# Performance work log

Measured on AMD Instinct MI355X. Metric: run time of the kernel, lower is better.

Reference implementation:

```python
import jax, jax.numpy as jnp
import numpy as np

B, T, E, H, VF, C = 4, 8192, 512, 8, 2, 256
KD = E // H          # key dim per head = 64
HD = E * VF // H     # value head dim = 128


def _rel_pos():
    decay = np.log(1.0 - 2.0 ** (-5.0 - np.arange(H, dtype=np.float64)))  # [H]
    ang = 1.0 / (10000 ** np.linspace(0, 1, KD // 2))
    ang = np.repeat(ang, 2)                                  # [KD]
    idx = np.arange(T)
    sin = np.sin(idx[:, None] * ang[None, :]).astype(np.float32)
    cos = np.cos(idx[:, None] * ang[None, :]).astype(np.float32)
    bi = np.arange(C)
    diff = bi[:, None] - bi[None, :]
    m = np.where(diff >= 0, np.exp(decay[:, None, None] * diff), 0.0)  # [H,C,C]
    last = m[:, -1]                                          # [H,C]
    vid = (last / last.sum(-1, keepdims=True))[:, :, None]   # [H,C,1]
    scale = np.sqrt(m.sum(-1, keepdims=True))                # [H,C,1]
    mask = (m / scale).astype(np.float32)
    cross_decay = np.exp(decay * C)[:, None, None].astype(np.float32)  # [H,1,1]
    qid = np.exp(decay[:, None] * (bi + 1))[:, :, None]      # [H,C,1]
    qid = (qid / (scale / last.sum(-1)[:, None, None])).astype(np.float32)
    return sin, cos, mask, cross_decay, qid, vid.astype(np.float32)


def setup_inputs() -> dict:
    key = jax.random.key(0)
    ks = jax.random.split(key, 6)
    sin, cos, mask, cross_decay, qid, vid = _rel_pos()
    s = 0.02
    return {
        'x': jax.random.normal(ks[0], (B, T, E), jnp.float32),
        'sin': jnp.asarray(sin), 'cos': jnp.asarray(cos),
        'mask': jnp.asarray(mask), 'cross_decay': jnp.asarray(cross_decay),
        'query_inner_decay': jnp.asarray(qid), 'value_inner_decay': jnp.asarray(vid),
        'Wq': jax.random.normal(ks[1], (E, E), jnp.float32) * s,
        'Wk': jax.random.normal(ks[2], (E, E), jnp.float32) * s,
        'Wv': jax.random.normal(ks[3], (E, E * VF), jnp.float32) * s,
        'Wg': jax.random.normal(ks[4], (E, E * VF), jnp.float32) * s,
        'Wo': jax.random.normal(ks[5], (E * VF, E), jnp.float32) * s,
    }


def _rotate_every_two(x):
    x1, x2 = x[..., ::2], x[..., 1::2]
    return jnp.stack((-x2, x1), axis=-1).reshape(x.shape)


def _theta_shift(x, sin, cos):
    return x * cos + _rotate_every_two(x) * sin


def reference(x, sin, cos, mask, cross_decay, query_inner_decay, value_inner_decay, Wq, Wk, Wv, Wg, Wo):
    Bz, Tl, _ = x.shape
    q = (x @ Wq).reshape(Bz, Tl, H, KD).transpose(0, 2, 1, 3)               # [B,H,T,KD]
    k = ((x @ Wk) * (KD ** -0.5)).reshape(Bz, Tl, H, KD).transpose(0, 2, 1, 3)
    v = x @ Wv                                                              # [B,T,E*VF]
    g = x @ Wg
    qr = _theta_shift(q, sin, cos)
    kr = _theta_shift(k, sin, cos)

    NC = Tl // C
    qr = qr.reshape(Bz, H, NC, C, KD).transpose(0, 2, 1, 3, 4)              # [B,NC,H,C,KD]
    kr = kr.reshape(Bz, H, NC, C, KD).transpose(0, 2, 1, 3, 4)
    vc = v.reshape(Bz, NC, C, H, HD).transpose(0, 1, 3, 2, 4)               # [B,NC,H,C,HD]

    qk = jnp.einsum('bnhck,bnhdk->bnhcd', qr, kr) * mask                    # decay-masked intra-chunk
    inner_scale = jnp.clip(jax.lax.stop_gradient(jnp.abs(qk)).sum(-1, keepdims=True), 1.0, None)
    qk = qk / inner_scale
    inner_output = jnp.einsum('bnhcd,bnhde->bnhce', qk, vc)                 # [B,NC,H,C,HD]

    kv = jnp.einsum('bnhck,bnhcd->bnhkd', kr, vc * value_inner_decay)       # [B,NC,H,KD,HD]

    def step(carry, kv_i):
        kv_state, kv_scale = carry
        out = (kv_state / kv_scale, kv_scale)
        kv_state = kv_state * cross_decay + kv_i
        kv_scale = jnp.clip(
            jax.lax.stop_gradient(jnp.abs(kv_state)).sum(-2, keepdims=True).max(-1, keepdims=True),
            1.0, None)
        return (kv_state, kv_scale), out

    kv_state0 = jnp.zeros((Bz, H, KD, HD), x.dtype)
    kv_scale0 = jnp.ones((Bz, H, 1, 1), x.dtype)
    _, (kv_recurrent, cross_scale) = jax.lax.scan(step, (kv_state0, kv_scale0), jnp.swapaxes(kv, 0, 1))
    kv_recurrent = jnp.swapaxes(kv_recurrent, 0, 1)                         # [B,NC,H,KD,HD]
    cross_scale = jnp.swapaxes(cross_scale, 0, 1)                           # [B,NC,H,1,1]

    all_scale = jnp.maximum(inner_scale, cross_scale)
    cross_output = jnp.einsum('bnhck,bnhkd->bnhcd', qr * query_inner_decay, kv_recurrent)
    output = inner_output / (all_scale / inner_scale) + cross_output / (all_scale / cross_scale)
    output = output.transpose(0, 1, 3, 2, 4)                                # [B,NC,C,H,HD]
    # group_norm: RMSNorm over head_dim, no affine
    output = output * jax.lax.rsqrt(jnp.mean(output ** 2, -1, keepdims=True) + 1e-6)
    output = output.reshape(Bz, Tl, H * HD)
    output = jax.nn.silu(g) * output
    return output @ Wo
```

## Files before the change

### kernel.cpp

```cpp
#include <hip/hip_runtime.h>
#include <hip/hip_bf16.h>
#include <cmath>

#define Bz 4
#define Tt 8192
#define Ee 512
#define Hh 8
#define Cc 256
#define KD 64
#define HD 128
#define NC 32
#define EV 1024
#define Mrows (Bz*Tt)

typedef unsigned short u16;
typedef __attribute__((ext_vector_type(4))) float f32x4;
typedef __attribute__((ext_vector_type(8))) short s16x8;

__device__ __forceinline__ u16 f2b(float f) {
    __hip_bfloat16 h = __float2bfloat16(f);
    return *reinterpret_cast<u16*>(&h);
}
__device__ __forceinline__ float b2f(u16 u) {
    union { unsigned u; float f; } v; v.u = ((unsigned)u) << 16;
    return v.f;
}
#define MFMA16(a, b, c) __builtin_amdgcn_mfma_f32_16x16x32_bf16((a), (b), (c), 0, 0, 0)

__device__ __forceinline__ void glds16(const u16* g, u16* l) {
    __builtin_amdgcn_global_load_lds(
        (const __attribute__((address_space(1))) unsigned int*)g,
        (__attribute__((address_space(3))) unsigned int*)l,
        16, 0, 0);
}

__device__ __forceinline__ size_t fpk(int row, int k, int K) {
    return (size_t)(row >> 4) * (K * 16) + (k >> 5) * 512 + ((k >> 3) & 3) * 128 +
           (row & 15) * 8 + (k & 7);
}

__global__ __launch_bounds__(256) void cast_x_k(const float* __restrict__ x,
                                                u16* __restrict__ xb) {
    size_t i = ((size_t)blockIdx.x * 256 + threadIdx.x) * 4;
    float4 v = *(const float4*)(x + i);
    int m = (int)(i >> 9), e = (int)(i & 511);
    ushort4 o;
    o.x = f2b(v.x); o.y = f2b(v.y); o.z = f2b(v.z); o.w = f2b(v.w);
    *(ushort4*)(xb + fpk(m, e, 512)) = o;
}

__global__ __launch_bounds__(256) void cast_mask_k(const float* __restrict__ m,
                                                   u16* __restrict__ mb) {
    size_t i = ((size_t)blockIdx.x * 256 + threadIdx.x) * 4;
    float4 v = *(const float4*)(m + i);
    ushort4 o;
    o.x = f2b(v.x); o.y = f2b(v.y); o.z = f2b(v.z); o.w = f2b(v.w);
    *(ushort4*)(mb + i) = o;
}

__global__ __launch_bounds__(256) void castT_k(const float* __restrict__ W,
                                               u16* __restrict__ Wt,
                                               int K, int N, float scale) {
    __shared__ float tile[32][33];
    int k0 = blockIdx.y * 32, n0 = blockIdx.x * 32;
    int r = threadIdx.x >> 3, c4 = (threadIdx.x & 7) * 4;
    float4 v = *(const float4*)(W + (size_t)(k0 + r) * N + n0 + c4);
    tile[r][c4] = v.x; tile[r][c4 + 1] = v.y; tile[r][c4 + 2] = v.z; tile[r][c4 + 3] = v.w;
    __syncthreads();
    ushort4 o;
    o.x = f2b(tile[c4 + 0][r] * scale);
    o.y = f2b(tile[c4 + 1][r] * scale);
    o.z = f2b(tile[c4 + 2][r] * scale);
    o.w = f2b(tile[c4 + 3][r] * scale);
    *(ushort4*)(Wt + fpk(n0 + r, k0 + c4, K)) = o;
}

template <int EPI>
__global__ __launch_bounds__(256) void gemm_mfma(const u16* __restrict__ A,
                                                 const u16* __restrict__ Bt,
                                                 void* __restrict__ Cout,
                                                 int K, int N,
                                                 const float* __restrict__ sn,
                                                 const float* __restrict__ cs) {
    __shared__ __align__(16) u16 pool[20480];
    u16 (*lds)[8192] = (u16(*)[8192])pool;
    int tid = threadIdx.x;
    int lane = tid & 63, wid = tid >> 6;
    int cL = lane & 15, quad = lane >> 4;
    int M0 = blockIdx.y * 8, N0 = blockIdx.x * 8;
    int m0 = blockIdx.y * 128 + (wid & 1) * 64;
    int n0 = blockIdx.x * 128 + (wid >> 1) * 64;
    const int KT = K * 16;
    const int NK = K >> 5;

#define STAGE(buf, kc) do {                                                        \
        size_t kofs = (size_t)(kc) * 512 + lane * 8;                               \
        glds16(A  + (size_t)(M0 + wid * 2    ) * KT + kofs,                        \
               &lds[buf][(wid * 2    ) * 512]);                                    \
        glds16(A  + (size_t)(M0 + wid * 2 + 1) * KT + kofs,                        \
               &lds[buf][(wid * 2 + 1) * 512]);                                    \
        glds16(Bt + (size_t)(N0 + wid * 2    ) * KT + kofs,                        \
               &lds[buf][4096 + (wid * 2    ) * 512]);                             \
        glds16(Bt + (size_t)(N0 + wid * 2 + 1) * KT + kofs,                        \
               &lds[buf][4096 + (wid * 2 + 1) * 512]);                             \
    } while (0)

    STAGE(0, 0);
    __syncthreads();

    f32x4 acc[4][4] = {};
    int mh = (wid & 1) * 4, nh = (wid >> 1) * 4;
    for (int kc = 0; kc < NK; ++kc) {
        int cur = kc & 1;
        if (kc + 1 < NK) STAGE(cur ^ 1, kc + 1);
        s16x8 af[4], bfr[4];
        int fo = quad * 128 + cL * 8;
        #pragma unroll
        for (int mt = 0; mt < 4; ++mt)
            af[mt] = *(const s16x8*)(&lds[cur][(mh + mt) * 512 + fo]);
        #pragma unroll
        for (int nt = 0; nt < 4; ++nt)
            bfr[nt] = *(const s16x8*)(&lds[cur][4096 + (nh + nt) * 512 + fo]);
        #pragma unroll
        for (int mt = 0; mt < 4; ++mt)
            #pragma unroll
            for (int nt = 0; nt < 4; ++nt)
                acc[mt][nt] = MFMA16(af[mt], bfr[nt], acc[mt][nt]);
        __syncthreads();
    }
#undef STAGE
    u16* ep = pool + wid * 5120;

    if (EPI == 0) {
        u16* dst = (u16*)Cout;
        int b = m0 >> 13, h = n0 >> 6, tb = m0 & 8191;
        #pragma unroll
        for (int mt = 0; mt < 4; ++mt)
            #pragma unroll
            for (int nt = 0; nt < 4; ++nt)
                #pragma unroll
                for (int i = 0; i < 4; ++i) {
                    int mrow = mt * 16 + quad * 4 + i;
                    int n = n0 + nt * 16 + cL;
                    float v = acc[mt][nt][i];
                    float p = __shfl_xor(v, 1, 64);
                    int t = tb + mrow, kd = n & 63;
                    float c1 = cs[t * 64 + kd], s1 = sn[t * 64 + kd];
                    float o = (n & 1) ? (v * c1 + p * s1) : (v * c1 - p * s1);
                    ep[mrow * 80 + nt * 16 + cL] = f2b(o);
                }
        u16* dstbh = dst + (size_t)(b * 8 + h) * 524288;
        #pragma unroll
        for (int g2 = 0; g2 < 4; ++g2)
            #pragma unroll
            for (int pass = 0; pass < 2; ++pass) {
                int kcol = pass * 32 + quad * 8;
                s16x8 vv = *(const s16x8*)(ep + (g2 * 16 + cL) * 80 + kcol);
                *(s16x8*)(dstbh + fpk(tb + g2 * 16 + cL, kcol, 64)) = vv;
            }
    } else if (EPI == 1) {
        u16* vt = (u16*)Cout;
        #pragma unroll
        for (int mt = 0; mt < 4; ++mt)
            #pragma unroll
            for (int nt = 0; nt < 4; ++nt) {
                int m = m0 + mt * 16 + quad * 4;
                int n = n0 + nt * 16 + cL;
                int b = m >> 13, t = m & 8191;
                int nn = t >> 8, ccc = t & 255;
                int h = n >> 7, e = n & 127;
                ushort4 pk;
                pk.x = f2b(acc[mt][nt][0]);
                pk.y = f2b(acc[mt][nt][1]);
                pk.z = f2b(acc[mt][nt][2]);
                pk.w = f2b(acc[mt][nt][3]);
                *(ushort4*)(vt + (((size_t)((b * 8 + h) * 32 + nn)) << 15) +
                            fpk(e, ccc, 256)) = pk;
            }
    } else if (EPI == 2) {
        u16* dst = (u16*)Cout;
        #pragma unroll
        for (int mt = 0; mt < 4; ++mt)
            #pragma unroll
            for (int nt = 0; nt < 4; ++nt)
                #pragma unroll
                for (int i = 0; i < 4; ++i)
                    ep[(mt * 16 + quad * 4 + i) * 80 + nt * 16 + cL] =
                        f2b(acc[mt][nt][i]);
        #pragma unroll
        for (int g2 = 0; g2 < 4; ++g2)
            #pragma unroll
            for (int pass = 0; pass < 2; ++pass) {
                int ncol = pass * 32 + quad * 8;
                s16x8 vv = *(const s16x8*)(ep + (g2 * 16 + cL) * 80 + ncol);
                *(s16x8*)(dst + fpk(m0 + g2 * 16 + cL, n0 + ncol, N)) = vv;
            }
    } else {
        float* dst = (float*)Cout;
        #pragma unroll
        for (int mt = 0; mt < 4; ++mt)
            #pragma unroll
            for (int nt = 0; nt < 4; ++nt)
                #pragma unroll
                for (int i = 0; i < 4; ++i)
                    dst[(size_t)(m0 + mt * 16 + quad * 4 + i) * N + n0 + nt * 16 + cL] =
                        acc[mt][nt][i];
    }
}

__global__ __launch_bounds__(256) void attn_mfma(const u16* __restrict__ qr,
                                                 const u16* __restrict__ kr,
                                                 const u16* __restrict__ vt,
                                                 const u16* __restrict__ maskb,
                                                 u16* __restrict__ ATT,
                                                 float* __restrict__ iscale_g) {
    __shared__ __align__(16) u16 Ss[64][264];
    __shared__ float partial[4][64];
    __shared__ float sInvL[64];
    int p = blockIdx.x;
    int g = (p & 7) | ((p >> 5) << 3);
    int rtile = (p >> 3) & 3;
    int h = g & 7; int n = (g >> 3) & 31; int b = g >> 8;
    int tid = threadIdx.x, lane = tid & 63, w = tid >> 6;
    int cL = lane & 15, quad = lane >> 4;

    size_t qf_bh = (size_t)(b * 8 + h) * 524288;
    f32x4 acc[4][4] = {};
    if (w <= rtile) {
        const u16* Qb = qr + qf_bh + (size_t)(n * 16 + rtile * 4) * 1024;
        const u16* Kb = kr + qf_bh + (size_t)(n * 16 + w * 4) * 1024;
        #pragma unroll
        for (int kt = 0; kt < 2; ++kt) {
            s16x8 af[4], bfr[4];
            size_t ko = (size_t)kt * 512 + quad * 128 + cL * 8;
            #pragma unroll
            for (int mt = 0; mt < 4; ++mt)
                af[mt] = *(const s16x8*)(Qb + (size_t)mt * 1024 + ko);
            #pragma unroll
            for (int nt = 0; nt < 4; ++nt)
                bfr[nt] = *(const s16x8*)(Kb + (size_t)nt * 1024 + ko);
            #pragma unroll
            for (int mt = 0; mt < 4; ++mt)
                #pragma unroll
                for (int nt = 0; nt < 4; ++nt)
                    acc[mt][nt] = MFMA16(af[mt], bfr[nt], acc[mt][nt]);
        }
    }
    float rs[4][4] = {};
    if (w <= rtile) {
        const u16* mb = maskb + ((size_t)h << 16);
        #pragma unroll
        for (int mt = 0; mt < 4; ++mt)
            #pragma unroll
            for (int nt = 0; nt < 4; ++nt)
                #pragma unroll
                for (int i = 0; i < 4; ++i) {
                    int r = rtile * 64 + mt * 16 + quad * 4 + i;
                    int d = w * 64 + nt * 16 + cL;
                    float s = acc[mt][nt][i] * b2f(mb[r * 256 + d]);
                    Ss[mt * 16 + quad * 4 + i][w * 64 + nt * 16 + cL] = f2b(s);
                    rs[mt][i] += fabsf(s);
                }
    }
    #pragma unroll
    for (int mt = 0; mt < 4; ++mt)
        #pragma unroll
        for (int i = 0; i < 4; ++i) {
            float v = rs[mt][i];
            v += __shfl_xor(v, 1, 16);
            v += __shfl_xor(v, 2, 16);
            v += __shfl_xor(v, 4, 16);
            v += __shfl_xor(v, 8, 16);
            if (cL == 0) partial[w][mt * 16 + quad * 4 + i] = v;
        }
    __syncthreads();
    if (tid < 64) {
        float tot = partial[0][tid] + partial[1][tid] + partial[2][tid] + partial[3][tid];
        tot = fmaxf(tot, 1.f);
        iscale_g[((size_t)((b * 32 + n) * 8 + h)) * 256 + rtile * 64 + tid] = tot;
        sInvL[tid] = 1.f / tot;
    }
    __syncthreads();

    f32x4 o[8] = {};
    const u16* Vb = vt + (((size_t)((b * 8 + h) * 32 + n)) << 15);
    int kmax = 2 * (rtile + 1);
    for (int kt = 0; kt < kmax; ++kt) {
        s16x8 a = *(const s16x8*)(&Ss[w * 16 + cL][kt * 32 + quad * 8]);
        #pragma unroll
        for (int nt = 0; nt < 8; ++nt) {
            s16x8 bv = *(const s16x8*)(Vb + (size_t)nt * 4096 + kt * 512 +
                                       quad * 128 + cL * 8);
            o[nt] = MFMA16(a, bv, o[nt]);
        }
    }
    #pragma unroll
    for (int nt = 0; nt < 8; ++nt)
        #pragma unroll
        for (int i = 0; i < 4; ++i) {
            int r = quad * 4 + i;
            Ss[w * 16 + r][nt * 16 + cL] = f2b(o[nt][i] * sInvL[w * 16 + r]);
        }
    size_t obase = ((size_t)b * 8192 + n * 256 + rtile * 64) * 1024 + h * 128;
    #pragma unroll
    for (int pass = 0; pass < 4; ++pass) {
        int e = pass * 32 + quad * 8;
        s16x8 vv = *(const s16x8*)(&Ss[w * 16 + cL][e]);
        *(s16x8*)(ATT + obase + (size_t)(w * 16 + cL) * 1024 + e) = vv;
    }
}

__global__ __launch_bounds__(256) void chunkkv_mfma(const u16* __restrict__ kr,
                                                    const u16* __restrict__ vt,
                                                    const float* __restrict__ vid,
                                                    float* __restrict__ kvT) {
    __shared__ u16 KtL[64][264];
    int bid = blockIdx.x;
    int h = bid & 7; bid >>= 3;
    int n = bid & 31; int b = bid >> 5;
    int tid = threadIdx.x, lane = tid & 63, w = tid >> 6;
    int cL = lane & 15, quad = lane >> 4;
    size_t qf_bh = (size_t)(b * 8 + h) * 524288;
    {
        int c = tid;
        const u16* rp = kr + qf_bh + (size_t)(n * 16 + (c >> 4)) * 1024 + (c & 15) * 8;
        #pragma unroll
        for (int u = 0; u < 8; ++u) {
            s16x8 vv = *(const s16x8*)(rp + (u >> 2) * 512 + (u & 3) * 128);
            #pragma unroll
            for (int j = 0; j < 8; ++j) KtL[u * 8 + j][c] = (u16)vv[j];
        }
    }
    __syncthreads();
    const u16* Vb = vt + (((size_t)((b * 8 + h) * 32 + n)) << 15);
    f32x4 acc[2][4] = {};
    for (int kt = 0; kt < 8; ++kt) {
        float vidv[8];
        #pragma unroll
        for (int j = 0; j < 8; ++j) vidv[j] = vid[h * 256 + kt * 32 + quad * 8 + j];
        s16x8 af[2];
        #pragma unroll
        for (int mt = 0; mt < 2; ++mt) {
            s16x8 raw = *(const s16x8*)(Vb + (size_t)(w * 2 + mt) * 4096 +
                                        kt * 512 + quad * 128 + cL * 8);
            #pragma unroll
            for (int j = 0; j < 8; ++j)
                af[mt][j] = (short)f2b(b2f((u16)raw[j]) * vidv[j]);
        }
        #pragma unroll
        for (int nt = 0; nt < 4; ++nt) {
            s16x8 bv = *(const s16x8*)(&KtL[nt * 16 + cL][kt * 32 + quad * 8]);
            #pragma unroll
            for (int mt = 0; mt < 2; ++mt) acc[mt][nt] = MFMA16(af[mt], bv, acc[mt][nt]);
        }
    }
    float* out = kvT + ((size_t)((b * 32 + n) * 8 + h)) * 8192;
    #pragma unroll
    for (int mt = 0; mt < 2; ++mt)
        #pragma unroll
        for (int nt = 0; nt < 4; ++nt)
            #pragma unroll
            for (int i = 0; i < 4; ++i)
                out[(w * 32 + mt * 16 + quad * 4 + i) * 64 + nt * 16 + cL] = acc[mt][nt][i];
}

__global__ __launch_bounds__(256) void scan_par(const float* __restrict__ kvT,
                                                u16* __restrict__ kvrecb,
                                                const float* __restrict__ cdv,
                                                float* __restrict__ cscale) {
    int bid = blockIdx.x;
    int n = bid & 31; bid >>= 5;
    int h = bid & 7; int b = bid >> 3;
    int tid = threadIdx.x, lane = tid & 63, g = tid >> 6;
    float cd = cdv[h];
    float st[32], cur[32], nxt[32];
    #pragma unroll
    for (int i = 0; i < 32; ++i) { st[i] = 0.f; nxt[i] = 0.f; }
    if (n > 0) {
        size_t base0 = ((size_t)((b * 32) * 8 + h)) * 8192;
        #pragma unroll
        for (int i = 0; i < 32; ++i) cur[i] = kvT[base0 + (g + 4 * i) * 64 + lane];
    }
    for (int j = 0; j < n; ++j) {
        if (j + 1 < n) {
            size_t basen = ((size_t)((b * 32 + j + 1) * 8 + h)) * 8192;
            #pragma unroll
            for (int i = 0; i < 32; ++i) nxt[i] = kvT[basen + (g + 4 * i) * 64 + lane];
        }
        #pragma unroll
        for (int i = 0; i < 32; ++i) st[i] = st[i] * cd + cur[i];
        #pragma unroll
        for (int i = 0; i < 32; ++i) cur[i] = nxt[i];
    }
    __shared__ float esum[128];
    __shared__ float sSc;
    #pragma unroll
    for (int i = 0; i < 32; ++i) {
        float s = fabsf(st[i]);
        s += __shfl_xor(s, 1, 64);
        s += __shfl_xor(s, 2, 64);
        s += __shfl_xor(s, 4, 64);
        s += __shfl_xor(s, 8, 64);
        s += __shfl_xor(s, 16, 64);
        s += __shfl_xor(s, 32, 64);
        if (lane == 0) esum[g + 4 * i] = s;
    }
    __syncthreads();
    if (tid < 64) {
        float m1 = fmaxf(esum[tid], esum[tid + 64]);
        m1 = fmaxf(m1, __shfl_xor(m1, 1, 64));
        m1 = fmaxf(m1, __shfl_xor(m1, 2, 64));
        m1 = fmaxf(m1, __shfl_xor(m1, 4, 64));
        m1 = fmaxf(m1, __shfl_xor(m1, 8, 64));
        m1 = fmaxf(m1, __shfl_xor(m1, 16, 64));
        m1 = fmaxf(m1, __shfl_xor(m1, 32, 64));
        if (tid == 0) sSc = fmaxf(m1, 1.f);
    }
    __syncthreads();
    float scale = sSc;
    float inv = 1.f / scale;
    size_t baseN = ((size_t)((b * 32 + n) * 8 + h)) * 8192;
    #pragma unroll
    for (int i = 0; i < 32; ++i) {
        int e = g + 4 * i;
        kvrecb[baseN + ((size_t)(lane >> 3) * 128 + e) * 8 + (lane & 7)] = f2b(st[i] * inv);
    }
    if (tid == 0) cscale[(b * 32 + n) * 8 + h] = scale;
}

__global__ __launch_bounds__(256) void cross_mfma(const u16* __restrict__ qr,
                                                  const u16* __restrict__ kvrecb,
                                                  const float* __restrict__ iscale_g,
                                                  const float* __restrict__ cscale_g,
                                                  const float* __restrict__ qid,
                                                  u16* __restrict__ ATT) {
    __shared__ __align__(16) u16 X[4][4608];
    int bid = blockIdx.x;
    int h = bid & 7; bid >>= 3;
    int n = bid & 31; int b = bid >> 5;
    int tid = threadIdx.x, lane = tid & 63, w = tid >> 6;
    int cL = lane & 15, quad = lane >> 4;
    size_t qf_bh = (size_t)(b * 8 + h) * 524288;
    const u16* Qb = qr + qf_bh + (size_t)(n * 16 + w * 4) * 1024;
    const u16* KVb = kvrecb + ((size_t)((b * 32 + n) * 8 + h)) * 8192;
    s16x8 af[4][2];
    #pragma unroll
    for (int mt = 0; mt < 4; ++mt)
        #pragma unroll
        for (int kt = 0; kt < 2; ++kt)
            af[mt][kt] = *(const s16x8*)(Qb + (size_t)mt * 1024 + kt * 512 +
                                         quad * 128 + cL * 8);
    float csc = cscale_g[(b * 32 + n) * 8 + h];
    size_t ibase = ((size_t)((b * 32 + n) * 8 + h)) * 256 + w * 64;
    size_t obase = ((size_t)(b * 8192 + n * 256 + w * 64)) * 1024 + h * 128;
    #pragma unroll
    for (int hn = 0; hn < 2; ++hn) {
        f32x4 acc[4][4] = {};
        #pragma unroll
        for (int kt = 0; kt < 2; ++kt)
            #pragma unroll
            for (int nt = 0; nt < 4; ++nt) {
                int e = (hn * 4 + nt) * 16 + cL;
                s16x8 bv = *(const s16x8*)(KVb + ((size_t)(kt * 4 + quad) * 128 + e) * 8);
                #pragma unroll
                for (int mt = 0; mt < 4; ++mt)
                    acc[mt][nt] = MFMA16(af[mt][kt], bv, acc[mt][nt]);
            }
        #pragma unroll
        for (int mt = 0; mt < 4; ++mt)
            #pragma unroll
            for (int i = 0; i < 4; ++i) {
                int r = mt * 16 + quad * 4 + i;
                float isc = iscale_g[ibase + r];
                float alls = fmaxf(isc, csc);
                float fC = (csc / alls) * qid[h * 256 + w * 64 + r];
                #pragma unroll
                for (int nt = 0; nt < 4; ++nt)
                    X[w][r * 72 + nt * 16 + cL] = f2b(acc[mt][nt][i] * fC);
            }
        #pragma unroll
        for (int g2 = 0; g2 < 4; ++g2)
            #pragma unroll
            for (int pass = 0; pass < 2; ++pass) {
                int r2 = g2 * 16 + cL;
                float isc2 = iscale_g[ibase + r2];
                float fI2 = isc2 / fmaxf(isc2, csc);
                int e = pass * 32 + quad * 8;
                s16x8 sv = *(const s16x8*)(&X[w][r2 * 72 + e]);
                size_t oi = obase + (size_t)r2 * 1024 + hn * 64 + e;
                s16x8 pv = *(const s16x8*)(ATT + oi);
                s16x8 ov;
                #pragma unroll
                for (int j = 0; j < 8; ++j)
                    ov[j] = (short)f2b(b2f((u16)pv[j]) * fI2 + b2f((u16)sv[j]));
                *(s16x8*)(ATT + oi) = ov;
            }
    }
}

__global__ __launch_bounds__(256) void rms_silu(const u16* __restrict__ ATT,
                                                u16* __restrict__ g) {
    __shared__ u16 att_s[16 * 1036];
    __shared__ float rmsv[16][8];
    int tile = blockIdx.x;
    int tid = threadIdx.x;
    size_t abase = (size_t)tile * 16 * 1024;
    int head = tid >> 5;
    #pragma unroll
    for (int jj = 0; jj < 16; ++jj) {
        ushort4 v = *(const ushort4*)(ATT + abase + (size_t)jj * 1024 + tid * 4);
        *(ushort4*)(att_s + jj * 1036 + tid * 4) = v;
        float x0 = b2f(v.x), x1 = b2f(v.y), x2 = b2f(v.z), x3 = b2f(v.w);
        float ss = x0 * x0 + x1 * x1 + x2 * x2 + x3 * x3;
        ss += __shfl_xor(ss, 1, 32);
        ss += __shfl_xor(ss, 2, 32);
        ss += __shfl_xor(ss, 4, 32);
        ss += __shfl_xor(ss, 8, 32);
        ss += __shfl_xor(ss, 16, 32);
        if ((tid & 31) == 0)
            rmsv[jj][head] = rsqrtf(ss * (1.f / 128.f) + 1e-6f);
    }
    __syncthreads();
    size_t gbase = (size_t)tile * 16384;
    #pragma unroll
    for (int it = 0; it < 16; ++it) {
        int p = it * 1024 + tid * 4;
        int e = ((p >> 9) << 5) | (((p >> 7) & 3) << 3) | (p & 7);
        int r = (p >> 3) & 15;
        ushort4 gv = *(const ushort4*)(g + gbase + p);
        ushort4 av = *(const ushort4*)(att_s + r * 1036 + e);
        float rms = rmsv[r][e >> 7];
        float x0 = b2f(av.x), x1 = b2f(av.y), x2 = b2f(av.z), x3 = b2f(av.w);
        float g0 = b2f(gv.x), g1 = b2f(gv.y), g2 = b2f(gv.z), g3 = b2f(gv.w);
        ushort4 ov;
        ov.x = f2b((g0 / (1.f + __expf(-g0))) * x0 * rms);
        ov.y = f2b((g1 / (1.f + __expf(-g1))) * x1 * rms);
        ov.z = f2b((g2 / (1.f + __expf(-g2))) * x2 * rms);
        ov.w = f2b((g3 / (1.f + __expf(-g3))) * x3 * rms);
        *(ushort4*)(g + gbase + p) = ov;
    }
}

extern "C" void kernel_launch(void* const* d_in, const int* in_sizes, int n_in,
                              void* d_out, int out_size, void* d_ws, size_t ws_size,
                              hipStream_t stream) {
    const float* x    = (const float*)d_in[0];
    const float* sn   = (const float*)d_in[1];
    const float* cs   = (const float*)d_in[2];
    const float* mask = (const float*)d_in[3];
    const float* cdv  = (const float*)d_in[4];
    const float* qid  = (const float*)d_in[5];
    const float* vid  = (const float*)d_in[6];
    const float* Wq   = (const float*)d_in[7];
    const float* Wk   = (const float*)d_in[8];
    const float* Wv   = (const float*)d_in[9];
    const float* Wg   = (const float*)d_in[10];
    const float* Wo   = (const float*)d_in[11];
    float* out = (float*)d_out;

    char* w = (char*)d_ws;
    u16* qr     = (u16*)w;   w += (size_t)16777216 * 2;
    u16* kr     = (u16*)w;   w += (size_t)16777216 * 2;
    u16* vt     = (u16*)w;   w += (size_t)33554432 * 2;
    u16* xbf    = (u16*)w;   w += (size_t)16777216 * 2;
    u16* wqT    = (u16*)w;   w += (size_t)262144 * 2;
    u16* wkT    = (u16*)w;   w += (size_t)262144 * 2;
    u16* wvT    = (u16*)w;   w += (size_t)524288 * 2;
    u16* wgT    = (u16*)w;   w += (size_t)524288 * 2;
    u16* woT    = (u16*)w;   w += (size_t)524288 * 2;
    float* kvT  = (float*)w; w += (size_t)8388608 * 4;
    u16* kvrecb = (u16*)w;   w += (size_t)8388608 * 2;
    float* iscale = (float*)w; w += (size_t)262144 * 4;
    float* cscale = (float*)w; w += (size_t)1024 * 4;
    u16* maskb  = (u16*)w;   w += (size_t)524288 * 2;

    u16* gbuf = qr;
    u16* ATT  = (u16*)d_out;

    dim3 blk(256);
    cast_x_k<<<dim3(16384), blk, 0, stream>>>(x, xbf);
    cast_mask_k<<<dim3(512), blk, 0, stream>>>(mask, maskb);
    castT_k<<<dim3(16, 16), blk, 0, stream>>>(Wq, wqT, 512, 512, 1.0f);
    castT_k<<<dim3(16, 16), blk, 0, stream>>>(Wk, wkT, 512, 512, 0.125f);
    castT_k<<<dim3(32, 16), blk, 0, stream>>>(Wv, wvT, 512, 1024, 1.0f);
    castT_k<<<dim3(32, 16), blk, 0, stream>>>(Wg, wgT, 512, 1024, 1.0f);
    castT_k<<<dim3(16, 32), blk, 0, stream>>>(Wo, woT, 1024, 512, 1.0f);
    gemm_mfma<0><<<dim3(4, 256), blk, 0, stream>>>(xbf, wqT, qr, 512, 512, sn, cs);
    gemm_mfma<0><<<dim3(4, 256), blk, 0, stream>>>(xbf, wkT, kr, 512, 512, sn, cs);
    gemm_mfma<1><<<dim3(8, 256), blk, 0, stream>>>(xbf, wvT, vt, 512, 1024, nullptr, nullptr);
    attn_mfma<<<dim3(4096), blk, 0, stream>>>(qr, kr, vt, maskb, ATT, iscale);
    chunkkv_mfma<<<dim3(1024), blk, 0, stream>>>(kr, vt, vid, kvT);
    scan_par<<<dim3(1024), blk, 0, stream>>>(kvT, kvrecb, cdv, cscale);
    cross_mfma<<<dim3(1024), blk, 0, stream>>>(qr, kvrecb, iscale, cscale, qid, ATT);
    gemm_mfma<2><<<dim3(8, 256), blk, 0, stream>>>(xbf, wgT, gbuf, 512, 1024, nullptr, nullptr);
    rms_silu<<<dim3(2048), blk, 0, stream>>>(ATT, gbuf);
    gemm_mfma<3><<<dim3(4, 256), blk, 0, stream>>>(gbuf, woT, out, 1024, 512, nullptr, nullptr);
}
```

Measured before the change: 642.7 us.

## Fuse QKV projections into one GEMM and fold cross-chunk output into attention

The Q, K and V projection GEMMs become a single launch over the concatenated transposed weights. The epilogue picks the rotary-to-qr/kr path or the chunked V layout based on the column range. The cross-chunk product (q times the recurrent KV state) is now computed inside the intra-chunk attention kernel and combined with the inner output before the single bf16 store. This removes the separate cross kernel, its read-modify-write pass over the attention buffer, and the iscale buffer. In exchange the attention kernel now runs after the scan, so it can no longer overlap with it, and it uses more registers for the extra accumulators.

```diff
diff --git a/kernel.cpp b/kernel.cpp
--- a/kernel.cpp
+++ b/kernel.cpp
@@ -75,15 +75,16 @@
     *(ushort4*)(Wt + fpk(n0 + r, k0 + c4, K)) = o;
 }
 
-template <int EPI>
-__global__ __launch_bounds__(256) void gemm_mfma(const u16* __restrict__ A,
+__global__ __launch_bounds__(256) void gemm_proj(const u16* __restrict__ A,
                                                  const u16* __restrict__ Bt,
-                                                 void* __restrict__ Cout,
-                                                 int K, int N,
+                                                 u16* __restrict__ qr,
+                                                 u16* __restrict__ kr,
+                                                 u16* __restrict__ vt,
                                                  const float* __restrict__ sn,
                                                  const float* __restrict__ cs) {
     __shared__ __align__(16) u16 pool[20480];
     u16 (*lds)[8192] = (u16(*)[8192])pool;
+    const int K = 512;
     int tid = threadIdx.x;
     int lane = tid & 63, wid = tid >> 6;
     int cL = lane & 15, quad = lane >> 4;
@@ -107,7 +108,6 @@
 
     STAGE(0, 0);
     __syncthreads();
-
     f32x4 acc[4][4] = {};
     int mh = (wid & 1) * 4, nh = (wid >> 1) * 4;
     for (int kc = 0; kc < NK; ++kc) {
@@ -131,9 +131,10 @@
 #undef STAGE
     u16* ep = pool + wid * 5120;
 
-    if (EPI == 0) {
-        u16* dst = (u16*)Cout;
-        int b = m0 >> 13, h = n0 >> 6, tb = m0 & 8191;
+    if (n0 < 1024) {
+        int b = m0 >> 13, tb = m0 & 8191;
+        int hq = (n0 & 511) >> 6;
+        u16* dstbh = (n0 < 512 ? qr : kr) + (size_t)(b * 8 + hq) * 524288;
         #pragma unroll
         for (int mt = 0; mt < 4; ++mt)
             #pragma unroll
@@ -149,7 +150,6 @@
                     float o = (n & 1) ? (v * c1 + p * s1) : (v * c1 - p * s1);
                     ep[mrow * 80 + nt * 16 + cL] = f2b(o);
                 }
-        u16* dstbh = dst + (size_t)(b * 8 + h) * 524288;
         #pragma unroll
         for (int g2 = 0; g2 < 4; ++g2)
             #pragma unroll
@@ -158,17 +158,16 @@
                 s16x8 vv = *(const s16x8*)(ep + (g2 * 16 + cL) * 80 + kcol);
                 *(s16x8*)(dstbh + fpk(tb + g2 * 16 + cL, kcol, 64)) = vv;
             }
-    } else if (EPI == 1) {
-        u16* vt = (u16*)Cout;
+    } else {
         #pragma unroll
         for (int mt = 0; mt < 4; ++mt)
             #pragma unroll
             for (int nt = 0; nt < 4; ++nt) {
                 int m = m0 + mt * 16 + quad * 4;
-                int n = n0 + nt * 16 + cL;
+                int nv = (n0 - 1024) + nt * 16 + cL;
                 int b = m >> 13, t = m & 8191;
                 int nn = t >> 8, ccc = t & 255;
-                int h = n >> 7, e = n & 127;
+                int h = nv >> 7, e = nv & 127;
                 ushort4 pk;
                 pk.x = f2b(acc[mt][nt][0]);
                 pk.y = f2b(acc[mt][nt][1]);
@@ -177,7 +176,63 @@
                 *(ushort4*)(vt + (((size_t)((b * 8 + h) * 32 + nn)) << 15) +
                             fpk(e, ccc, 256)) = pk;
             }
-    } else if (EPI == 2) {
+    }
+}
+
+template <int EPI>
+__global__ __launch_bounds__(256) void gemm_mfma(const u16* __restrict__ A,
+                                                 const u16* __restrict__ Bt,
+                                                 void* __restrict__ Cout,
+                                                 int K, int N) {
+    __shared__ __align__(16) u16 pool[20480];
+    u16 (*lds)[8192] = (u16(*)[8192])pool;
+    int tid = threadIdx.x;
+    int lane = tid & 63, wid = tid >> 6;
+    int cL = lane & 15, quad = lane >> 4;
+    int M0 = blockIdx.y * 8, N0 = blockIdx.x * 8;
+    int m0 = blockIdx.y * 128 + (wid & 1) * 64;
+    int n0 = blockIdx.x * 128 + (wid >> 1) * 64;
+    const int KT = K * 16;
+    const int NK = K >> 5;
+
+#define STAGE(buf, kc) do {                                                        \
+        size_t kofs = (size_t)(kc) * 512 + lane * 8;                               \
+        glds16(A  + (size_t)(M0 + wid * 2    ) * KT + kofs,                        \
+               &lds[buf][(wid * 2    ) * 512]);                                    \
+        glds16(A  + (size_t)(M0 + wid * 2 + 1) * KT + kofs,                        \
+               &lds[buf][(wid * 2 + 1) * 512]);                                    \
+        glds16(Bt + (size_t)(N0 + wid * 2    ) * KT + kofs,                        \
+               &lds[buf][4096 + (wid * 2    ) * 512]);                             \
+        glds16(Bt + (size_t)(N0 + wid * 2 + 1) * KT + kofs,                        \
+               &lds[buf][4096 + (wid * 2 + 1) * 512]);                             \
+    } while (0)
+
+    STAGE(0, 0);
+    __syncthreads();
+    f32x4 acc[4][4] = {};
+    int mh = (wid & 1) * 4, nh = (wid >> 1) * 4;
+    for (int kc = 0; kc < NK; ++kc) {
+        int cur = kc & 1;
+        if (kc + 1 < NK) STAGE(cur ^ 1, kc + 1);
+        s16x8 af[4], bfr[4];
+        int fo = quad * 128 + cL * 8;
+        #pragma unroll
+        for (int mt = 0; mt < 4; ++mt)
+            af[mt] = *(const s16x8*)(&lds[cur][(mh + mt) * 512 + fo]);
+        #pragma unroll
+        for (int nt = 0; nt < 4; ++nt)
+            bfr[nt] = *(const s16x8*)(&lds[cur][4096 + (nh + nt) * 512 + fo]);
+        #pragma unroll
+        for (int mt = 0; mt < 4; ++mt)
+            #pragma unroll
+            for (int nt = 0; nt < 4; ++nt)
+                acc[mt][nt] = MFMA16(af[mt], bfr[nt], acc[mt][nt]);
+        __syncthreads();
+    }
+#undef STAGE
+    u16* ep = pool + wid * 5120;
+
+    if (EPI == 2) {
         u16* dst = (u16*)Cout;
         #pragma unroll
         for (int mt = 0; mt < 4; ++mt)
@@ -208,15 +263,17 @@
     }
 }
 
-__global__ __launch_bounds__(256) void attn_mfma(const u16* __restrict__ qr,
-                                                 const u16* __restrict__ kr,
-                                                 const u16* __restrict__ vt,
-                                                 const u16* __restrict__ maskb,
-                                                 u16* __restrict__ ATT,
-                                                 float* __restrict__ iscale_g) {
+__global__ __launch_bounds__(256) void attn_cross(const u16* __restrict__ qr,
+                                                  const u16* __restrict__ kr,
+                                                  const u16* __restrict__ vt,
+                                                  const u16* __restrict__ maskb,
+                                                  const u16* __restrict__ kvrecb,
+                                                  const float* __restrict__ cscale_g,
+                                                  const float* __restrict__ qid,
+                                                  u16* __restrict__ ATT) {
     __shared__ __align__(16) u16 Ss[64][264];
     __shared__ float partial[4][64];
-    __shared__ float sInvL[64];
+    __shared__ float sIsc[64];
     int p = blockIdx.x;
     int g = (p & 7) | ((p >> 5) << 3);
     int rtile = (p >> 3) & 3;
@@ -276,9 +333,7 @@
     __syncthreads();
     if (tid < 64) {
         float tot = partial[0][tid] + partial[1][tid] + partial[2][tid] + partial[3][tid];
-        tot = fmaxf(tot, 1.f);
-        iscale_g[((size_t)((b * 32 + n) * 8 + h)) * 256 + rtile * 64 + tid] = tot;
-        sInvL[tid] = 1.f / tot;
+        sIsc[tid] = fmaxf(tot, 1.f);
     }
     __syncthreads();
 
@@ -294,13 +349,37 @@
             o[nt] = MFMA16(a, bv, o[nt]);
         }
     }
-    #pragma unroll
-    for (int nt = 0; nt < 8; ++nt)
-        #pragma unroll
-        for (int i = 0; i < 4; ++i) {
-            int r = quad * 4 + i;
-            Ss[w * 16 + r][nt * 16 + cL] = f2b(o[nt][i] * sInvL[w * 16 + r]);
-        }
+
+    f32x4 acc2[8] = {};
+    {
+        const u16* Qc = qr + qf_bh + (size_t)(n * 16 + rtile * 4 + w) * 1024;
+        const u16* KVb = kvrecb + ((size_t)((b * 32 + n) * 8 + h)) * 8192;
+        s16x8 afc[2];
+        afc[0] = *(const s16x8*)(Qc + quad * 128 + cL * 8);
+        afc[1] = *(const s16x8*)(Qc + 512 + quad * 128 + cL * 8);
+        #pragma unroll
+        for (int kt = 0; kt < 2; ++kt)
+            #pragma unroll
+            for (int nt = 0; nt < 8; ++nt) {
+                s16x8 bv = *(const s16x8*)(KVb +
+                            ((size_t)(kt * 4 + quad) * 128 + nt * 16 + cL) * 8);
+                acc2[nt] = MFMA16(afc[kt], bv, acc2[nt]);
+            }
+    }
+
+    float csc = cscale_g[(b * 32 + n) * 8 + h];
+    #pragma unroll
+    for (int i = 0; i < 4; ++i) {
+        int rloc = w * 16 + quad * 4 + i;
+        float isc = sIsc[rloc];
+        float alls = fmaxf(isc, csc);
+        float invA = 1.f / alls;
+        float fC = csc * invA * qid[h * 256 + rtile * 64 + rloc];
+        #pragma unroll
+        for (int nt = 0; nt < 8; ++nt)
+            Ss[w * 16 + quad * 4 + i][nt * 16 + cL] =
+                f2b(o[nt][i] * invA + acc2[nt][i] * fC);
+    }
     size_t obase = ((size_t)b * 8192 + n * 256 + rtile * 64) * 1024 + h * 128;
     #pragma unroll
     for (int pass = 0; pass < 4; ++pass) {
@@ -426,76 +505,6 @@
         kvrecb[baseN + ((size_t)(lane >> 3) * 128 + e) * 8 + (lane & 7)] = f2b(st[i] * inv);
     }
     if (tid == 0) cscale[(b * 32 + n) * 8 + h] = scale;
-}
-
-__global__ __launch_bounds__(256) void cross_mfma(const u16* __restrict__ qr,
-                                                  const u16* __restrict__ kvrecb,
-                                                  const float* __restrict__ iscale_g,
-                                                  const float* __restrict__ cscale_g,
-                                                  const float* __restrict__ qid,
-                                                  u16* __restrict__ ATT) {
-    __shared__ __align__(16) u16 X[4][4608];
-    int bid = blockIdx.x;
-    int h = bid & 7; bid >>= 3;
-    int n = bid & 31; int b = bid >> 5;
-    int tid = threadIdx.x, lane = tid & 63, w = tid >> 6;
-    int cL = lane & 15, quad = lane >> 4;
-    size_t qf_bh = (size_t)(b * 8 + h) * 524288;
-    const u16* Qb = qr + qf_bh + (size_t)(n * 16 + w * 4) * 1024;
-    const u16* KVb = kvrecb + ((size_t)((b * 32 + n) * 8 + h)) * 8192;
-    s16x8 af[4][2];
-    #pragma unroll
-    for (int mt = 0; mt < 4; ++mt)
-        #pragma unroll
-        for (int kt = 0; kt < 2; ++kt)
-            af[mt][kt] = *(const s16x8*)(Qb + (size_t)mt * 1024 + kt * 512 +
-                                         quad * 128 + cL * 8);
-    float csc = cscale_g[(b * 32 + n) * 8 + h];
-    size_t ibase = ((size_t)((b * 32 + n) * 8 + h)) * 256 + w * 64;
-    size_t obase = ((size_t)(b * 8192 + n * 256 + w * 64)) * 1024 + h * 128;
-    #pragma unroll
-    for (int hn = 0; hn < 2; ++hn) {
-        f32x4 acc[4][4] = {};
-        #pragma unroll
-        for (int kt = 0; kt < 2; ++kt)
-            #pragma unroll
-            for (int nt = 0; nt < 4; ++nt) {
-                int e = (hn * 4 + nt) * 16 + cL;
-                s16x8 bv = *(const s16x8*)(KVb + ((size_t)(kt * 4 + quad) * 128 + e) * 8);
-                #pragma unroll
-                for (int mt = 0; mt < 4; ++mt)
-                    acc[mt][nt] = MFMA16(af[mt][kt], bv, acc[mt][nt]);
-            }
-        #pragma unroll
-        for (int mt = 0; mt < 4; ++mt)
-            #pragma unroll
-            for (int i = 0; i < 4; ++i) {
-                int r = mt * 16 + quad * 4 + i;
-                float isc = iscale_g[ibase + r];
-                float alls = fmaxf(isc, csc);
-                float fC = (csc / alls) * qid[h * 256 + w * 64 + r];
-                #pragma unroll
-                for (int nt = 0; nt < 4; ++nt)
-                    X[w][r * 72 + nt * 16 + cL] = f2b(acc[mt][nt][i] * fC);
-            }
-        #pragma unroll
-        for (int g2 = 0; g2 < 4; ++g2)
-            #pragma unroll
-            for (int pass = 0; pass < 2; ++pass) {
-                int r2 = g2 * 16 + cL;
-                float isc2 = iscale_g[ibase + r2];
-                float fI2 = isc2 / fmaxf(isc2, csc);
-                int e = pass * 32 + quad * 8;
-                s16x8 sv = *(const s16x8*)(&X[w][r2 * 72 + e]);
-                size_t oi = obase + (size_t)r2 * 1024 + hn * 64 + e;
-                s16x8 pv = *(const s16x8*)(ATT + oi);
-                s16x8 ov;
-                #pragma unroll
-                for (int j = 0; j < 8; ++j)
-                    ov[j] = (short)f2b(b2f((u16)pv[j]) * fI2 + b2f((u16)sv[j]));
-                *(s16x8*)(ATT + oi) = ov;
-            }
-    }
 }
 
 __global__ __launch_bounds__(256) void rms_silu(const u16* __restrict__ ATT,
@@ -570,7 +579,6 @@
     u16* woT    = (u16*)w;   w += (size_t)524288 * 2;
     float* kvT  = (float*)w; w += (size_t)8388608 * 4;
     u16* kvrecb = (u16*)w;   w += (size_t)8388608 * 2;
-    float* iscale = (float*)w; w += (size_t)262144 * 4;
     float* cscale = (float*)w; w += (size_t)1024 * 4;
     u16* maskb  = (u16*)w;   w += (size_t)524288 * 2;
 
@@ -585,14 +593,12 @@
     castT_k<<<dim3(32, 16), blk, 0, stream>>>(Wv, wvT, 512, 1024, 1.0f);
     castT_k<<<dim3(32, 16), blk, 0, stream>>>(Wg, wgT, 512, 1024, 1.0f);
     castT_k<<<dim3(16, 32), blk, 0, stream>>>(Wo, woT, 1024, 512, 1.0f);
-    gemm_mfma<0><<<dim3(4, 256), blk, 0, stream>>>(xbf, wqT, qr, 512, 512, sn, cs);
-    gemm_mfma<0><<<dim3(4, 256), blk, 0, stream>>>(xbf, wkT, kr, 512, 512, sn, cs);
-    gemm_mfma<1><<<dim3(8, 256), blk, 0, stream>>>(xbf, wvT, vt, 512, 1024, nullptr, nullptr);
-    attn_mfma<<<dim3(4096), blk, 0, stream>>>(qr, kr, vt, maskb, ATT, iscale);
+    gemm_proj<<<dim3(16, 256), blk, 0, stream>>>(xbf, wqT, qr, kr, vt, sn, cs);
     chunkkv_mfma<<<dim3(1024), blk, 0, stream>>>(kr, vt, vid, kvT);
     scan_par<<<dim3(1024), blk, 0, stream>>>(kvT, kvrecb, cdv, cscale);
-    cross_mfma<<<dim3(1024), blk, 0, stream>>>(qr, kvrecb, iscale, cscale, qid, ATT);
-    gemm_mfma<2><<<dim3(8, 256), blk, 0, stream>>>(xbf, wgT, gbuf, 512, 1024, nullptr, nullptr);
+    attn_cross<<<dim3(4096), blk, 0, stream>>>(qr, kr, vt, maskb, kvrecb, cscale,
+                                               qid, ATT);
+    gemm_mfma<2><<<dim3(8, 256), blk, 0, stream>>>(xbf, wgT, gbuf, 512, 1024);
     rms_silu<<<dim3(2048), blk, 0, stream>>>(ATT, gbuf);
-    gemm_mfma<3><<<dim3(4, 256), blk, 0, stream>>>(gbuf, woT, out, 1024, 512, nullptr, nullptr);
-}
+    gemm_mfma<3><<<dim3(4, 256), blk, 0, stream>>>(gbuf, woT, out, 1024, 512);
+}
```

New measurement: 589.6 us. -8.3%, faster.
